# Optimization experiments

Hardware: AMD Instinct MI355X
Metric: run time of the kernel (lower is better)

Reference implementation:

```python
import jax, jax.numpy as jnp
import numpy as np

B, S, D, H, DFF = 2, 2048, 1024, 16, 4096
DK = D // H


def _layer_norm(x, g, b, eps=1e-5):
    mu = jnp.mean(x, axis=-1, keepdims=True)
    var = jnp.mean((x - mu) ** 2, axis=-1, keepdims=True)
    return (x - mu) / jnp.sqrt(var + eps) * g + b


def setup_inputs() -> dict:
    key = jax.random.key(0)
    ks = jax.random.split(key, 12)
    w = lambda k, shape: jax.random.normal(k, shape, jnp.float32) * 0.02
    return {
        "x": jax.random.normal(ks[0], (B, S, D), jnp.float32),
        "mask": jnp.tril(jnp.ones((1, 1, S, S), jnp.int32)),  # causal tgt mask
        "Wq": w(ks[1], (D, D)), "bq": jnp.zeros((D,), jnp.float32),
        "Wk": w(ks[2], (D, D)), "bk": jnp.zeros((D,), jnp.float32),
        "Wv": w(ks[3], (D, D)), "bv": jnp.zeros((D,), jnp.float32),
        "Wo": w(ks[4], (D, D)), "bo": jnp.zeros((D,), jnp.float32),
        "W1": w(ks[5], (D, DFF)), "b1": jnp.zeros((DFF,), jnp.float32),
        "W2": w(ks[6], (DFF, D)), "b2": jnp.zeros((D,), jnp.float32),
        "g1": jnp.ones((D,), jnp.float32), "be1": jnp.zeros((D,), jnp.float32),
        "g2": jnp.ones((D,), jnp.float32), "be2": jnp.zeros((D,), jnp.float32),
    }


def reference(x, mask, Wq, bq, Wk, bk, Wv, bv, Wo, bo, W1, b1, W2, b2, g1, be1, g2, be2):
    b, s, d = x.shape
    h, dk = H, DK
    split = lambda t: t.reshape(b, s, h, dk).transpose(0, 2, 1, 3)  # [b,h,s,dk]
    q = split(x @ Wq + bq)
    k = split(x @ Wk + bk)
    v = split(x @ Wv + bv)
    scores = jnp.einsum("bhqd,bhkd->bhqk", q, k) / jnp.sqrt(jnp.float32(dk))
    # ALiBi: slope_h = (2**(8/H))**-(h+1); bias[h,i,j] = slope_h * (j - i)
    slopes = (2.0 ** (8.0 / h)) ** (-jnp.arange(1, h + 1, dtype=jnp.float32))
    rel = (jnp.arange(s)[None, :] - jnp.arange(s)[:, None]).astype(jnp.float32)
    scores = scores + slopes[:, None, None] * rel[None]  # [1? broadcast b,h,s,s]
    scores = jnp.where(mask == 0, jnp.float32(-1e9), scores)
    probs = jax.nn.softmax(scores, axis=-1)
    attn = jnp.einsum("bhqk,bhkd->bhqd", probs, v)
    attn = attn.transpose(0, 2, 1, 3).reshape(b, s, d) @ Wo + bo
    x = _layer_norm(x + attn, g1, be1)
    ff = jax.nn.relu(x @ W1 + b1) @ W2 + b2
    return _layer_norm(x + ff, g2, be2)
```

## Files before the change

### kernel.cpp

```cpp
#include <hip/hip_runtime.h>
#include <stdint.h>

typedef unsigned short u16;
typedef __bf16 bf16x8 __attribute__((ext_vector_type(8)));
typedef float f32x4 __attribute__((ext_vector_type(4)));
typedef float f32x16 __attribute__((ext_vector_type(16)));
typedef unsigned int uint2v __attribute__((ext_vector_type(2)));

#define S_LEN 2048
#define D_MODEL 1024

struct TrueT  { static constexpr bool value = true;  };
struct FalseT { static constexpr bool value = false; };

__device__ __forceinline__ u16 f2b(float f) {
    uint32_t u = __float_as_uint(f);
    u += 0x7FFFu + ((u >> 16) & 1u);
    return (u16)(u >> 16);
}

__device__ __forceinline__ uint32_t pk2(float a, float b) {
    union { struct { __bf16 l, h; } s; uint32_t u; } c;
    c.s.l = (__bf16)a; c.s.h = (__bf16)b; return c.u;
}

__device__ __forceinline__ float fexp2(float x) {
#if __has_builtin(__builtin_amdgcn_exp2f)
    return __builtin_amdgcn_exp2f(x);
#else
    return exp2f(x);
#endif
}

__device__ __forceinline__ uint2v plswap(uint32_t a, uint32_t b) {
#if __has_builtin(__builtin_amdgcn_permlane32_swap)
    return __builtin_amdgcn_permlane32_swap(a, b, false, false);
#else
    uint2v r;
    uint32_t pa = (uint32_t)__shfl_xor((int)a, 32, 64);
    uint32_t pb = (uint32_t)__shfl_xor((int)b, 32, 64);
    const int hi = (threadIdx.x & 63) >> 5;
    r[0] = hi ? pb : a;
    r[1] = hi ? b : pa;
    return r;
#endif
}
__device__ __forceinline__ float xhalf_max(float x) {
    uint2v r = plswap(__float_as_uint(x), __float_as_uint(x));
    return fmaxf(__uint_as_float(r[0]), __uint_as_float(r[1]));
}
__device__ __forceinline__ float xhalf_add(float x) {
    uint2v r = plswap(__float_as_uint(x), __float_as_uint(x));
    return __uint_as_float(r[0]) + __uint_as_float(r[1]);
}

__device__ __forceinline__ void gl16(const void* g, void* l) {
    __builtin_amdgcn_global_load_lds(
        (const __attribute__((address_space(1))) void*)g,
        (__attribute__((address_space(3))) void*)l, 16, 0, 0);
}

__global__ __launch_bounds__(256) void k_convert_bf16(
    const float* __restrict__ in, u16* __restrict__ out, int n)
{
    int i = (blockIdx.x * 256 + threadIdx.x) * 4;
    if (i >= n) return;
    float4 v = *reinterpret_cast<const float4*>(in + i);
    ushort4 o;
    o.x = f2b(v.x); o.y = f2b(v.y); o.z = f2b(v.z); o.w = f2b(v.w);
    *reinterpret_cast<ushort4*>(out + i) = o;
}

__global__ __launch_bounds__(256) void k_transpose_w(
    const float* __restrict__ W, u16* __restrict__ WT, int K, int N)
{
    __shared__ float tile[32][33];
    const int nt = blockIdx.x, kt = blockIdx.y;
    const int tx = threadIdx.x & 31, ty = threadIdx.x >> 5;
#pragma unroll
    for (int i = 0; i < 4; ++i)
        tile[ty + i * 8][tx] = W[(long)(kt * 32 + ty + i * 8) * N + nt * 32 + tx];
    __syncthreads();
#pragma unroll
    for (int i = 0; i < 4; ++i)
        WT[(long)(nt * 32 + ty + i * 8) * K + kt * 32 + tx] = f2b(tile[tx][ty + i * 8]);
}

template <int MODE>
__global__ __launch_bounds__(256) void k_gemm(
    const u16* __restrict__ A, const u16* __restrict__ BT,
    const float* __restrict__ bias, const float* __restrict__ bias2,
    const float* __restrict__ bias3,
    u16* __restrict__ outb, float* __restrict__ outf,
    int M, int N, int K, int va, int vb)
{
    __shared__ u16 As[2][128 * 32];
    __shared__ u16 Bs[2][128 * 32];
    const int t = threadIdx.x;
    const int lane = t & 63, wid = t >> 6;
    const int wm = wid >> 1, wn = wid & 1;
    const int lr = lane & 15, lg = lane >> 4;

    const int GX = gridDim.x, GY = gridDim.y;
    const int dd = blockIdx.y * GX + blockIdx.x;
    const int xcd = dd & 7, ii = dd >> 3;
    const int hb = GY / va, wb = GX / vb;
    const int pr = xcd / vb, pc = xcd % vb;
    const int by = pr * hb + ii / wb;
    const int bx = pc * wb + ii % wb;
    const int m0 = by * 128, n0 = bx * 128;

    const int Kc = K / (int)gridDim.z;
    const long koff = (long)blockIdx.z * Kc;

    f32x4 acc[4][4];
#pragma unroll
    for (int i = 0; i < 4; ++i)
#pragma unroll
        for (int j = 0; j < 4; ++j) acc[i][j] = (f32x4){0.f, 0.f, 0.f, 0.f};

    const int r0 = t >> 2;
    const int ce = (t & 3) * 8;
    const u16* pA0 = A + (long)(m0 + r0) * K + ce + koff;
    const u16* pA1 = A + (long)(m0 + r0 + 64) * K + ce + koff;
    const u16* pB0 = BT + (long)(n0 + r0) * K + ce + koff;
    const u16* pB1 = BT + (long)(n0 + r0 + 64) * K + ce + koff;

    auto STAGE = [&](int buf, int k0) {
        u16* aw = &As[buf][wid * 512];
        u16* bw = &Bs[buf][wid * 512];
        gl16(pA0 + k0, aw);
        gl16(pA1 + k0, aw + 2048);
        gl16(pB0 + k0, bw);
        gl16(pB1 + k0, bw + 2048);
    };

    STAGE(0, 0);
    __syncthreads();
    int cur = 0;
    for (int k0 = 0; k0 < Kc; k0 += 32) {
        if (k0 + 32 < Kc) STAGE(cur ^ 1, k0 + 32);
        bf16x8 af[4], bfr[4];
#pragma unroll
        for (int i = 0; i < 4; ++i)
            af[i] = *reinterpret_cast<const bf16x8*>(&As[cur][(wm * 64 + i * 16 + lr) * 32 + lg * 8]);
#pragma unroll
        for (int j = 0; j < 4; ++j)
            bfr[j] = *reinterpret_cast<const bf16x8*>(&Bs[cur][(wn * 64 + j * 16 + lr) * 32 + lg * 8]);
#pragma unroll
        for (int i = 0; i < 4; ++i)
#pragma unroll
            for (int j = 0; j < 4; ++j)
                acc[i][j] = __builtin_amdgcn_mfma_f32_16x16x32_bf16(af[i], bfr[j], acc[i][j], 0, 0, 0);
        __syncthreads();
        cur ^= 1;
    }

    const long zoff = (long)blockIdx.z * M * N;
#pragma unroll
    for (int i = 0; i < 4; ++i) {
#pragma unroll
        for (int j = 0; j < 4; ++j) {
            const int n = n0 + wn * 64 + j * 16 + lr;
            float bn = 0.f;
            if (MODE == 0)
                bn = (n < 1024) ? bias[n] : (n < 2048) ? bias2[n - 1024] : bias3[n - 2048];
            else if (MODE == 2)
                bn = bias[n];
#pragma unroll
            for (int r = 0; r < 4; ++r) {
                const int m = m0 + wm * 64 + i * 16 + lg * 4 + r;
                float v = acc[i][j][r] + bn;
                if (MODE == 0) {
                    const int b = m >> 11, s = m & 2047;
                    const int which = n >> 10, nn = n & 1023;
                    const int h = nn >> 6, dk = nn & 63;
                    const long bhb = (long)(b * 16 + h) * (2048L * 64);
                    const int s32 = s >> 5, sr = s & 31;
                    long addr;
                    if (which < 2) {
                        addr = bhb + (long)s32 * 2048 + (dk >> 4) * 512 +
                               ((dk >> 3) & 1) * 256 + sr * 8 + (dk & 7);
                    } else {
                        addr = bhb + (long)s32 * 2048 + (dk >> 5) * 1024 +
                               ((sr >> 4) & 1) * 512 + ((sr >> 3) & 1) * 256 +
                               (dk & 31) * 8 + (sr & 7);
                    }
                    outb[(long)which * (32L * 2048 * 64) + addr] = f2b(v);
                } else if (MODE == 2) {
                    outb[(long)m * N + n] = f2b(fmaxf(v, 0.f));
                } else {
                    outf[zoff + (long)m * N + n] = v;
                }
            }
        }
    }
}

__global__ __launch_bounds__(512, 2) void k_gemm8(
    const u16* __restrict__ A, const u16* __restrict__ BT,
    const float* __restrict__ bias, u16* __restrict__ outb,
    int M, int N, int K, int va, int vb)
{
    __shared__ u16 As[2][2][8192];
    __shared__ u16 Bs[2][2][8192];
    const int t = threadIdx.x;
    const int lane = t & 63, wid = t >> 6;
    const int wm = wid >> 2, wn = wid & 3;
    const int lr = lane & 15, lg = lane >> 4;

    const int GX = gridDim.x, GY = gridDim.y;
    const int dd = blockIdx.y * GX + blockIdx.x;
    const int xcd = dd & 7, ii = dd >> 3;
    const int hb = GY / va, wb = GX / vb;
    const int by = (xcd / vb) * hb + ii / wb;
    const int bx = (xcd % vb) * wb + ii % wb;
    const int m0 = by * 256, n0 = bx * 256;

    const int NT = K >> 6;

    auto STAGEU = [&](const u16* __restrict__ P, int rbase, u16* lds_unit,
                      int tt, int kh) {
        const int ko = tt * 64 + kh * 32;
#pragma unroll
        for (int s = 0; s < 2; ++s) {
            const int c = wid * 64 + lane + s * 512;
            const int op = c * 16;
            const int row = op >> 6;
            const int kg = ((op >> 4) & 3) ^ ((row >> 1) & 3);
            gl16(P + (long)(rbase + row) * K + ko + kg * 8,
                 (char*)lds_unit + op);
        }
    };
    auto RD = [&](const u16* unit, int rb) -> bf16x8 {
        const int row = rb + lr;
        const int op = (row * 64 + lg * 16) ^ (((row >> 1) & 3) << 4);
        return *reinterpret_cast<const bf16x8*>((const char*)unit + op);
    };

    f32x4 acc[8][4];
#pragma unroll
    for (int i = 0; i < 8; ++i)
#pragma unroll
        for (int j = 0; j < 4; ++j) acc[i][j] = (f32x4){0.f, 0.f, 0.f, 0.f};

    STAGEU(A, m0, &As[0][0][0], 0, 0);
    STAGEU(BT, n0, &Bs[0][0][0], 0, 0);
    STAGEU(A, m0, &As[0][1][0], 0, 1);
    STAGEU(BT, n0, &Bs[0][1][0], 0, 1);
    STAGEU(A, m0, &As[1][0][0], 1, 0);
    STAGEU(BT, n0, &Bs[1][0][0], 1, 0);
    asm volatile("s_waitcnt vmcnt(0)" ::: "memory");
    __builtin_amdgcn_s_barrier();

    for (int tt = 0; tt < NT; ++tt) {
        const int sl = tt & 1;
        bf16x8 af[4], bfr[4];

#pragma unroll
        for (int rf = 0; rf < 4; ++rf)
            af[rf] = RD(&As[sl][0][0], wm * 128 + rf * 16);
#pragma unroll
        for (int cf = 0; cf < 4; ++cf)
            bfr[cf] = RD(&Bs[sl][0][0], wn * 64 + cf * 16);
        if (tt + 1 < NT) STAGEU(A, m0, &As[sl ^ 1][1][0], tt + 1, 1);
        __builtin_amdgcn_s_setprio(1);
#pragma unroll
        for (int cf = 0; cf < 4; ++cf)
#pragma unroll
            for (int rf = 0; rf < 4; ++rf)
                acc[rf][cf] = __builtin_amdgcn_mfma_f32_16x16x32_bf16(af[rf], bfr[cf], acc[rf][cf], 0, 0, 0);
        __builtin_amdgcn_s_setprio(0);
        __builtin_amdgcn_s_barrier();

#pragma unroll
        for (int rf = 0; rf < 4; ++rf)
            af[rf] = RD(&As[sl][0][0], wm * 128 + 64 + rf * 16);
        if (tt + 1 < NT) STAGEU(BT, n0, &Bs[sl ^ 1][1][0], tt + 1, 1);
        __builtin_amdgcn_s_setprio(1);
#pragma unroll
        for (int cf = 0; cf < 4; ++cf)
#pragma unroll
            for (int rf = 0; rf < 4; ++rf)
                acc[4 + rf][cf] = __builtin_amdgcn_mfma_f32_16x16x32_bf16(af[rf], bfr[cf], acc[4 + rf][cf], 0, 0, 0);
        __builtin_amdgcn_s_setprio(0);
        asm volatile("s_waitcnt vmcnt(8)" ::: "memory");
        __builtin_amdgcn_s_barrier();

#pragma unroll
        for (int rf = 0; rf < 4; ++rf)
            af[rf] = RD(&As[sl][1][0], wm * 128 + rf * 16);
#pragma unroll
        for (int cf = 0; cf < 4; ++cf)
            bfr[cf] = RD(&Bs[sl][1][0], wn * 64 + cf * 16);
        if (tt + 2 < NT) STAGEU(A, m0, &As[sl][0][0], tt + 2, 0);
        __builtin_amdgcn_s_setprio(1);
#pragma unroll
        for (int cf = 0; cf < 4; ++cf)
#pragma unroll
            for (int rf = 0; rf < 4; ++rf)
                acc[rf][cf] = __builtin_amdgcn_mfma_f32_16x16x32_bf16(af[rf], bfr[cf], acc[rf][cf], 0, 0, 0);
        __builtin_amdgcn_s_setprio(0);
        __builtin_amdgcn_s_barrier();

#pragma unroll
        for (int rf = 0; rf < 4; ++rf)
            af[rf] = RD(&As[sl][1][0], wm * 128 + 64 + rf * 16);
        if (tt + 2 < NT) STAGEU(BT, n0, &Bs[sl][0][0], tt + 2, 0);
        __builtin_amdgcn_s_setprio(1);
#pragma unroll
        for (int cf = 0; cf < 4; ++cf)
#pragma unroll
            for (int rf = 0; rf < 4; ++rf)
                acc[4 + rf][cf] = __builtin_amdgcn_mfma_f32_16x16x32_bf16(af[rf], bfr[cf], acc[4 + rf][cf], 0, 0, 0);
        __builtin_amdgcn_s_setprio(0);
        asm volatile("s_waitcnt vmcnt(8)" ::: "memory");
        __builtin_amdgcn_s_barrier();
    }

#pragma unroll
    for (int fr = 0; fr < 8; ++fr)
#pragma unroll
        for (int cf = 0; cf < 4; ++cf) {
            const int n = n0 + wn * 64 + cf * 16 + lr;
            const float bn = bias[n];
#pragma unroll
            for (int r = 0; r < 4; ++r) {
                const int m = m0 + wm * 128 + fr * 16 + lg * 4 + r;
                outb[(long)m * N + n] = f2b(fmaxf(acc[fr][cf][r] + bn, 0.f));
            }
        }
}

__global__ __launch_bounds__(512, 2) void k_gemm8n(
    const u16* __restrict__ A, const u16* __restrict__ BT,
    float* __restrict__ outf, int M, int N, int K, int va, int vb)
{
    __shared__ u16 As[2][2][8192];
    __shared__ u16 Bs[2][2][4096];
    const int t = threadIdx.x;
    const int lane = t & 63, wid = t >> 6;
    const int wm = wid >> 1, wn = wid & 1;
    const int lr = lane & 15, lg = lane >> 4;

    const int GX = gridDim.x, GY = gridDim.y;
    const int dd = blockIdx.y * GX + blockIdx.x;
    const int xcd = dd & 7, ii = dd >> 3;
    const int hb = GY / va, wb = GX / vb;
    const int by = (xcd / vb) * hb + ii / wb;
    const int bx = (xcd % vb) * wb + ii % wb;
    const int m0 = by * 256, n0 = bx * 128;

    const int Kc = K / (int)gridDim.z;
    const long koff = (long)blockIdx.z * Kc;
    const int NT = Kc >> 6;

    auto STAGEA = [&](u16* lds_unit, int tt, int kh) {
        const int ko = tt * 64 + kh * 32;
#pragma unroll
        for (int s = 0; s < 2; ++s) {
            const int c = wid * 64 + lane + s * 512;
            const int op = c * 16;
            const int row = op >> 6;
            const int kg = ((op >> 4) & 3) ^ ((row >> 1) & 3);
            gl16(A + (long)(m0 + row) * K + koff + ko + kg * 8,
                 (char*)lds_unit + op);
        }
    };
    auto STAGEB = [&](u16* lds_unit, int tt, int kh) {
        const int ko = tt * 64 + kh * 32;
        const int c = wid * 64 + lane;
        const int op = c * 16;
        const int row = op >> 6;
        const int kg = ((op >> 4) & 3) ^ ((row >> 1) & 3);
        gl16(BT + (long)(n0 + row) * K + koff + ko + kg * 8,
             (char*)lds_unit + op);
    };
    auto RD = [&](const u16* unit, int rb) -> bf16x8 {
        const int row = rb + lr;
        const int op = (row * 64 + lg * 16) ^ (((row >> 1) & 3) << 4);
        return *reinterpret_cast<const bf16x8*>((const char*)unit + op);
    };

    f32x4 acc[4][4];
#pragma unroll
    for (int i = 0; i < 4; ++i)
#pragma unroll
        for (int j = 0; j < 4; ++j) acc[i][j] = (f32x4){0.f, 0.f, 0.f, 0.f};

    STAGEA(&As[0][0][0], 0, 0); STAGEB(&Bs[0][0][0], 0, 0);
    STAGEA(&As[0][1][0], 0, 1); STAGEB(&Bs[0][1][0], 0, 1);
    STAGEA(&As[1][0][0], 1, 0); STAGEB(&Bs[1][0][0], 1, 0);
    asm volatile("s_waitcnt vmcnt(0)" ::: "memory");
    __builtin_amdgcn_s_barrier();

    for (int tt = 0; tt < NT; ++tt) {
        const int sl = tt & 1;
        bf16x8 af[4], bfr[4];

#pragma unroll
        for (int rf = 0; rf < 4; ++rf)
            af[rf] = RD(&As[sl][0][0], wm * 64 + rf * 16);
#pragma unroll
        for (int cf = 0; cf < 4; ++cf)
            bfr[cf] = RD(&Bs[sl][0][0], wn * 64 + cf * 16);
        if (tt + 1 < NT) {
            STAGEA(&As[sl ^ 1][1][0], tt + 1, 1);
            STAGEB(&Bs[sl ^ 1][1][0], tt + 1, 1);
        }
        __builtin_amdgcn_s_setprio(1);
#pragma unroll
        for (int cf = 0; cf < 4; ++cf)
#pragma unroll
            for (int rf = 0; rf < 4; ++rf)
                acc[rf][cf] = __builtin_amdgcn_mfma_f32_16x16x32_bf16(af[rf], bfr[cf], acc[rf][cf], 0, 0, 0);
        __builtin_amdgcn_s_setprio(0);
        asm volatile("s_waitcnt vmcnt(6)" ::: "memory");
        __builtin_amdgcn_s_barrier();

#pragma unroll
        for (int rf = 0; rf < 4; ++rf)
            af[rf] = RD(&As[sl][1][0], wm * 64 + rf * 16);
#pragma unroll
        for (int cf = 0; cf < 4; ++cf)
            bfr[cf] = RD(&Bs[sl][1][0], wn * 64 + cf * 16);
        if (tt + 2 < NT) {
            STAGEA(&As[sl][0][0], tt + 2, 0);
            STAGEB(&Bs[sl][0][0], tt + 2, 0);
        }
        __builtin_amdgcn_s_setprio(1);
#pragma unroll
        for (int cf = 0; cf < 4; ++cf)
#pragma unroll
            for (int rf = 0; rf < 4; ++rf)
                acc[rf][cf] = __builtin_amdgcn_mfma_f32_16x16x32_bf16(af[rf], bfr[cf], acc[rf][cf], 0, 0, 0);
        __builtin_amdgcn_s_setprio(0);
        asm volatile("s_waitcnt vmcnt(6)" ::: "memory");
        __builtin_amdgcn_s_barrier();
    }

    const long zoff = (long)blockIdx.z * M * N;
#pragma unroll
    for (int fr = 0; fr < 4; ++fr)
#pragma unroll
        for (int cf = 0; cf < 4; ++cf) {
            const int n = n0 + wn * 64 + cf * 16 + lr;
#pragma unroll
            for (int r = 0; r < 4; ++r) {
                const int m = m0 + wm * 64 + fr * 16 + lg * 4 + r;
                outf[zoff + (long)m * N + n] = acc[fr][cf][r];
            }
        }
}

__global__ __launch_bounds__(256, 3) void k_attn4(
    const u16* __restrict__ qg, const u16* __restrict__ kg,
    const u16* __restrict__ vtg, u16* __restrict__ attnb)
{
    __shared__ float Ol[4][32][68];
    __shared__ float Ml[4][32];
    __shared__ float Ll[4][32];

    const int t = threadIdx.x;
    const int lane = t & 63, w = t >> 6;
    const int qc = lane & 31, hi = lane >> 5;
    const int bid = blockIdx.x;
    const int xcd = bid & 7, slot = bid >> 3;
    const int bh = xcd * 4 + (slot & 3);
    const int pr = slot >> 2;
    const int b = bh >> 4, h = bh & 15;
    const float slope2 = fexp2(-0.5f * (float)(h + 1)) * 1.44269504f;
    const float SC = 0.18033688f;
    const long base = (long)bh * (S_LEN * 64L);

    const u16* kptr = kg + base + lane * 8;
    const u16* vptr = vtg + base + lane * 8;
    const u16* qptr = qg + base + lane * 8;

#define LOADK(S, DST) {                                                   \
        const u16* kr_ = kptr + (long)(S) * 2048;                         \
        DST[0] = *reinterpret_cast<const bf16x8*>(kr_);                   \
        DST[1] = *reinterpret_cast<const bf16x8*>(kr_ + 512);             \
        DST[2] = *reinterpret_cast<const bf16x8*>(kr_ + 1024);            \
        DST[3] = *reinterpret_cast<const bf16x8*>(kr_ + 1536); }

    for (int pi = 0; pi < 2; ++pi) {
        const int qt = pi ? pr : 63 - pr;
        const int q_abs = qt * 32 + qc;

        bf16x8 qf[4];
        {
            const u16* qt_ = qptr + (long)qt * 2048;
#pragma unroll
            for (int ds = 0; ds < 4; ++ds)
                qf[ds] = *reinterpret_cast<const bf16x8*>(qt_ + ds * 512);
        }

        f32x16 oacc[2];
#pragma unroll
        for (int i = 0; i < 16; ++i) { oacc[0][i] = 0.f; oacc[1][i] = 0.f; }
        float m = -1e30f, l = 0.f;

        const int nsub = qt + 1;
        const int L = (nsub + 3) >> 2;
        const int s_beg = w * L;
        const int s_end = min(s_beg + L, nsub);
        const bool has_diag = (s_beg < s_end) && (s_end == nsub);
        const int e_un = has_diag ? s_end - 1 : s_end;

        bf16x8 kf[4];

        auto SUBTILE = [&](int s, int nxt, auto MASKC) {
            constexpr bool MASK = decltype(MASKC)::value;
            const int k0 = s * 32;
            f32x16 st;
#pragma unroll
            for (int i = 0; i < 16; ++i) st[i] = 0.f;
#pragma unroll
            for (int ds = 0; ds < 4; ++ds)
                st = __builtin_amdgcn_mfma_f32_32x32x16_bf16(kf[ds], qf[ds], st, 0, 0, 0);
            if (nxt >= 0) LOADK(nxt, kf);
            bf16x8 vf[2][2];
            {
                const u16* vt_ = vptr + (long)s * 2048;
#pragma unroll
                for (int dh = 0; dh < 2; ++dh)
#pragma unroll
                    for (int ks = 0; ks < 2; ++ks)
                        vf[dh][ks] = *reinterpret_cast<const bf16x8*>(
                            vt_ + dh * 1024 + ks * 512);
            }

            const float b0 = slope2 * (float)(k0 - q_abs + 4 * hi);
#pragma unroll
            for (int r = 0; r < 16; ++r) {
                const int roff = (r & 3) + 8 * (r >> 2);
                float xx = fmaf(st[r], SC, fmaf((float)roff, slope2, b0));
                if (MASK) {
                    const int kabs = k0 + roff + 4 * hi;
                    xx = (kabs > q_abs) ? -1e30f : xx;
                }
                st[r] = xx;
            }
            float mt[8];
#pragma unroll
            for (int r = 0; r < 8; ++r) mt[r] = fmaxf(st[2 * r], st[2 * r + 1]);
#pragma unroll
            for (int r = 0; r < 4; ++r) mt[r] = fmaxf(mt[r], mt[r + 4]);
            mt[0] = fmaxf(mt[0], mt[2]); mt[1] = fmaxf(mt[1], mt[3]);
            float mloc = xhalf_max(fmaxf(mt[0], mt[1]));

            if (!__all(mloc <= m + 11.5416f)) {
                const float mnew = fmaxf(m, mloc);
                const float corr = fexp2(m - mnew);
                m = mnew;
                l *= corr;
#pragma unroll
                for (int i = 0; i < 16; ++i) { oacc[0][i] *= corr; oacc[1][i] *= corr; }
            }

#pragma unroll
            for (int r = 0; r < 16; ++r) st[r] = fexp2(st[r] - m);
            float pt[8];
#pragma unroll
            for (int r = 0; r < 8; ++r) pt[r] = st[2 * r] + st[2 * r + 1];
#pragma unroll
            for (int r = 0; r < 4; ++r) pt[r] = pt[r] + pt[r + 4];
            pt[0] += pt[2]; pt[1] += pt[3];
            l += xhalf_add(pt[0] + pt[1]);

            bf16x8 pa[2];
#pragma unroll
            for (int g2 = 0; g2 < 2; ++g2) {
                uint32_t o0 = pk2(st[8 * g2 + 0], st[8 * g2 + 1]);
                uint32_t o1 = pk2(st[8 * g2 + 2], st[8 * g2 + 3]);
                uint32_t o2 = pk2(st[8 * g2 + 4], st[8 * g2 + 5]);
                uint32_t o3 = pk2(st[8 * g2 + 6], st[8 * g2 + 7]);
                uint2v ra = plswap(o0, o2);
                uint2v rb = plswap(o1, o3);
                union { uint32_t wd[4]; bf16x8 v; } c;
                c.wd[0] = ra[0]; c.wd[1] = rb[0]; c.wd[2] = ra[1]; c.wd[3] = rb[1];
                pa[g2] = c.v;
            }
#pragma unroll
            for (int ks = 0; ks < 2; ++ks)
#pragma unroll
                for (int dh = 0; dh < 2; ++dh)
                    oacc[dh] = __builtin_amdgcn_mfma_f32_32x32x16_bf16(vf[dh][ks], pa[ks], oacc[dh], 0, 0, 0);
        };

        int s = s_beg;
        if (s < s_end) LOADK(s, kf);
        for (; s < e_un; ++s)
            SUBTILE(s, (s + 1 < s_end) ? s + 1 : -1, FalseT{});
        if (has_diag)
            SUBTILE(qt, -1, TrueT{});

#pragma unroll
        for (int dh = 0; dh < 2; ++dh)
#pragma unroll
            for (int g = 0; g < 4; ++g) {
                float4 o4 = make_float4(oacc[dh][4 * g + 0], oacc[dh][4 * g + 1],
                                        oacc[dh][4 * g + 2], oacc[dh][4 * g + 3]);
                *reinterpret_cast<float4*>(&Ol[w][qc][dh * 32 + g * 8 + hi * 4]) = o4;
            }
        if (hi == 0) { Ml[w][qc] = m; Ll[w][qc] = l; }
        __syncthreads();

        {
            const int q = t >> 3, dg = t & 7;
            const float m0v = Ml[0][q], m1v = Ml[1][q], m2v = Ml[2][q], m3v = Ml[3][q];
            const float M = fmaxf(fmaxf(m0v, m1v), fmaxf(m2v, m3v));
            float wgt[4];
            wgt[0] = fexp2(m0v - M); wgt[1] = fexp2(m1v - M);
            wgt[2] = fexp2(m2v - M); wgt[3] = fexp2(m3v - M);
            const float lsum = wgt[0] * Ll[0][q] + wgt[1] * Ll[1][q] +
                               wgt[2] * Ll[2][q] + wgt[3] * Ll[3][q];
            float acc8[8];
#pragma unroll
            for (int e = 0; e < 8; ++e) acc8[e] = 0.f;
#pragma unroll
            for (int w4 = 0; w4 < 4; ++w4) {
                const float wg = wgt[w4];
#pragma unroll
                for (int e = 0; e < 8; ++e)
                    acc8[e] += wg * Ol[w4][q][dg * 8 + e];
            }
            const float inv = 1.0f / lsum;
            u16 ob[8];
#pragma unroll
            for (int e = 0; e < 8; ++e) ob[e] = f2b(acc8[e] * inv);
            *reinterpret_cast<uint4*>(
                &attnb[((long)b * S_LEN + qt * 32 + q) * 1024 + h * 64 + dg * 8]) =
                *reinterpret_cast<uint4*>(&ob[0]);
        }
        __syncthreads();
    }
#undef LOADK
}

__global__ __launch_bounds__(256) void k_ln(
    const float* __restrict__ P0, const float* __restrict__ P1,
    const float* __restrict__ resid, const float* __restrict__ pbias,
    const float* __restrict__ g, const float* __restrict__ be,
    float* __restrict__ outf, u16* __restrict__ outb, int writeb)
{
    __shared__ float red[2][4];
    const int row = blockIdx.x, t = threadIdx.x;
    const long o = (long)row * 1024 + t * 4;
    float4 a0 = *reinterpret_cast<const float4*>(P0 + o);
    float4 a1 = *reinterpret_cast<const float4*>(P1 + o);
    float4 rr = *reinterpret_cast<const float4*>(resid + o);
    float4 pb = *reinterpret_cast<const float4*>(pbias + t * 4);
    float4 vv;
    vv.x = a0.x + a1.x + rr.x + pb.x;
    vv.y = a0.y + a1.y + rr.y + pb.y;
    vv.z = a0.z + a1.z + rr.z + pb.z;
    vv.w = a0.w + a1.w + rr.w + pb.w;
    float s = vv.x + vv.y + vv.z + vv.w;
    float sq = vv.x * vv.x + vv.y * vv.y + vv.z * vv.z + vv.w * vv.w;
#pragma unroll
    for (int off = 1; off < 64; off <<= 1) {
        s += __shfl_xor(s, off, 64);
        sq += __shfl_xor(sq, off, 64);
    }
    const int w = t >> 6;
    if ((t & 63) == 0) { red[0][w] = s; red[1][w] = sq; }
    __syncthreads();
    s = red[0][0] + red[0][1] + red[0][2] + red[0][3];
    sq = red[1][0] + red[1][1] + red[1][2] + red[1][3];
    const float mu = s * (1.f / 1024.f);
    const float var = sq * (1.f / 1024.f) - mu * mu;
    const float rs = rsqrtf(var + 1e-5f);
    float4 gv = *reinterpret_cast<const float4*>(&g[t * 4]);
    float4 bv = *reinterpret_cast<const float4*>(&be[t * 4]);
    float4 ov;
    ov.x = (vv.x - mu) * rs * gv.x + bv.x;
    ov.y = (vv.y - mu) * rs * gv.y + bv.y;
    ov.z = (vv.z - mu) * rs * gv.z + bv.z;
    ov.w = (vv.w - mu) * rs * gv.w + bv.w;
    *reinterpret_cast<float4*>(&outf[o]) = ov;
    if (writeb) {
        ushort4 ob;
        ob.x = f2b(ov.x); ob.y = f2b(ov.y); ob.z = f2b(ov.z); ob.w = f2b(ov.w);
        *reinterpret_cast<ushort4*>(&outb[o]) = ob;
    }
}

extern "C" void kernel_launch(void* const* d_in, const int* in_sizes, int n_in,
                              void* d_out, int out_size, void* d_ws, size_t ws_size,
                              hipStream_t stream)
{
    const float* x  = (const float*)d_in[0];
    const float* Wq = (const float*)d_in[2];  const float* bq = (const float*)d_in[3];
    const float* Wk = (const float*)d_in[4];  const float* bk = (const float*)d_in[5];
    const float* Wv = (const float*)d_in[6];  const float* bv = (const float*)d_in[7];
    const float* Wo = (const float*)d_in[8];  const float* bo = (const float*)d_in[9];
    const float* W1 = (const float*)d_in[10]; const float* b1 = (const float*)d_in[11];
    const float* W2 = (const float*)d_in[12]; const float* b2 = (const float*)d_in[13];
    const float* g1 = (const float*)d_in[14]; const float* be1 = (const float*)d_in[15];
    const float* g2 = (const float*)d_in[16]; const float* be2 = (const float*)d_in[17];
    float* out = (float*)d_out;

    char* ws = (char*)d_ws;
    const size_t MB = 1 << 20;
    u16* XB   = (u16*)(ws + 0 * MB);
    u16* QKVT = (u16*)(ws + 8 * MB);
    u16* WOT  = (u16*)(ws + 14 * MB);
    u16* W1T  = (u16*)(ws + 16 * MB);
    u16* W2T  = (u16*)(ws + 96 * MB);
    u16* QKV  = (u16*)(ws + 32 * MB);
    u16* AT   = (u16*)(ws + 64 * MB);
    float* OP = (float*)(ws + 32 * MB);
    float* Y1 = (float*)(ws + 0 * MB);
    u16* Y1B  = (u16*)(ws + 64 * MB);
    u16* Hb   = (u16*)(ws + 24 * MB);
    float* FP = (float*)(ws + 56 * MB);

    u16* Qb = QKV;
    u16* Kb = QKV + 32L * 2048 * 64;
    u16* Vb = QKV + 2 * 32L * 2048 * 64;

    dim3 blk(256);

    k_convert_bf16<<<dim3(4096), blk, 0, stream>>>(x, XB, 4096 * 1024);
    k_transpose_w<<<dim3(32, 32), blk, 0, stream>>>(Wq, QKVT, 1024, 1024);
    k_transpose_w<<<dim3(32, 32), blk, 0, stream>>>(Wk, QKVT + 1024L * 1024, 1024, 1024);
    k_transpose_w<<<dim3(32, 32), blk, 0, stream>>>(Wv, QKVT + 2048L * 1024, 1024, 1024);
    k_transpose_w<<<dim3(32, 32), blk, 0, stream>>>(Wo, WOT, 1024, 1024);
    k_transpose_w<<<dim3(128, 32), blk, 0, stream>>>(W1, W1T, 1024, 4096);
    k_transpose_w<<<dim3(32, 128), blk, 0, stream>>>(W2, W2T, 4096, 1024);

    k_gemm<0><<<dim3(24, 32), blk, 0, stream>>>(XB, QKVT, bq, bk, bv,
                                                QKV, nullptr, 4096, 3072, 1024, 4, 2);

    k_attn4<<<dim3(1024), blk, 0, stream>>>(Qb, Kb, Vb, AT);

    k_gemm8n<<<dim3(8, 16, 2), dim3(512), 0, stream>>>(AT, WOT, OP,
                                                       4096, 1024, 1024, 2, 4);
    k_ln<<<dim3(4096), blk, 0, stream>>>(OP, OP + 4096L * 1024, x, bo,
                                         g1, be1, Y1, Y1B, 1);
    k_gemm8<<<dim3(16, 16), dim3(512), 0, stream>>>(Y1B, W1T, b1, Hb,
                                                    4096, 4096, 1024, 2, 4);
    k_gemm8n<<<dim3(8, 16, 2), dim3(512), 0, stream>>>(Hb, W2T, FP,
                                                       4096, 1024, 4096, 2, 4);
    k_ln<<<dim3(4096), blk, 0, stream>>>(FP, FP + 4096L * 1024, Y1, b2,
                                         g2, be2, out, nullptr, 0);
}
```

Measured before the change: 222.9 us.

## Use 256x256 split-K=4 GEMM for FFN down-projection with bf16 partials

The W2 GEMM moves from the 256x128 split-K=2 kernel to the 256x256 tile kernel, now templated to support split-K over gridDim.z. It writes four bf16 partial planes with no bias. A new LayerNorm kernel sums the four bf16 partials with the residual and bias before normalizing. The aim is better operand reuse from the larger tile, plus half-width partial traffic in exchange for extra partial planes, at the cost of precision loss from rounding the partials to bf16.

```diff
diff --git a/kernel.cpp b/kernel.cpp
--- a/kernel.cpp
+++ b/kernel.cpp
@@ -17,6 +17,11 @@
     uint32_t u = __float_as_uint(f);
     u += 0x7FFFu + ((u >> 16) & 1u);
     return (u16)(u >> 16);
+}
+
+__device__ __forceinline__ float b2f(u16 b) {
+    uint32_t u = (uint32_t)b << 16;
+    return __uint_as_float(u);
 }
 
 __device__ __forceinline__ uint32_t pk2(float a, float b) {
@@ -197,6 +202,7 @@
     }
 }
 
+template <int MODE>
 __global__ __launch_bounds__(512, 2) void k_gemm8(
     const u16* __restrict__ A, const u16* __restrict__ BT,
     const float* __restrict__ bias, u16* __restrict__ outb,
@@ -217,7 +223,9 @@
     const int bx = (xcd % vb) * wb + ii % wb;
     const int m0 = by * 256, n0 = bx * 256;
 
-    const int NT = K >> 6;
+    const int Kc = K / (int)gridDim.z;
+    const long koff = (long)blockIdx.z * Kc;
+    const int NT = Kc >> 6;
 
     auto STAGEU = [&](const u16* __restrict__ P, int rbase, u16* lds_unit,
                       int tt, int kh) {
@@ -228,7 +236,7 @@
             const int op = c * 16;
             const int row = op >> 6;
             const int kg = ((op >> 4) & 3) ^ ((row >> 1) & 3);
-            gl16(P + (long)(rbase + row) * K + ko + kg * 8,
+            gl16(P + (long)(rbase + row) * K + koff + ko + kg * 8,
                  (char*)lds_unit + op);
         }
     };
@@ -318,16 +326,20 @@
         __builtin_amdgcn_s_barrier();
     }
 
+    const long zoff = (long)blockIdx.z * M * N;
 #pragma unroll
     for (int fr = 0; fr < 8; ++fr)
 #pragma unroll
         for (int cf = 0; cf < 4; ++cf) {
             const int n = n0 + wn * 64 + cf * 16 + lr;
-            const float bn = bias[n];
+            const float bn = (MODE == 0) ? bias[n] : 0.f;
 #pragma unroll
             for (int r = 0; r < 4; ++r) {
                 const int m = m0 + wm * 128 + fr * 16 + lg * 4 + r;
-                outb[(long)m * N + n] = f2b(fmaxf(acc[fr][cf][r] + bn, 0.f));
+                if (MODE == 0)
+                    outb[(long)m * N + n] = f2b(fmaxf(acc[fr][cf][r] + bn, 0.f));
+                else
+                    outb[zoff + (long)m * N + n] = f2b(acc[fr][cf][r]);
             }
         }
 }
@@ -687,6 +699,51 @@
     }
 }
 
+__global__ __launch_bounds__(256) void k_ln4b(
+    const u16* __restrict__ P, long plane,
+    const float* __restrict__ resid, const float* __restrict__ pbias,
+    const float* __restrict__ g, const float* __restrict__ be,
+    float* __restrict__ outf)
+{
+    __shared__ float red[2][4];
+    const int row = blockIdx.x, t = threadIdx.x;
+    const long o = (long)row * 1024 + t * 4;
+    float4 rr = *reinterpret_cast<const float4*>(resid + o);
+    float4 pb = *reinterpret_cast<const float4*>(pbias + t * 4);
+    float4 vv;
+    vv.x = rr.x + pb.x; vv.y = rr.y + pb.y;
+    vv.z = rr.z + pb.z; vv.w = rr.w + pb.w;
+#pragma unroll
+    for (int z = 0; z < 4; ++z) {
+        ushort4 p4 = *reinterpret_cast<const ushort4*>(P + z * plane + o);
+        vv.x += b2f(p4.x); vv.y += b2f(p4.y);
+        vv.z += b2f(p4.z); vv.w += b2f(p4.w);
+    }
+    float s = vv.x + vv.y + vv.z + vv.w;
+    float sq = vv.x * vv.x + vv.y * vv.y + vv.z * vv.z + vv.w * vv.w;
+#pragma unroll
+    for (int off = 1; off < 64; off <<= 1) {
+        s += __shfl_xor(s, off, 64);
+        sq += __shfl_xor(sq, off, 64);
+    }
+    const int w = t >> 6;
+    if ((t & 63) == 0) { red[0][w] = s; red[1][w] = sq; }
+    __syncthreads();
+    s = red[0][0] + red[0][1] + red[0][2] + red[0][3];
+    sq = red[1][0] + red[1][1] + red[1][2] + red[1][3];
+    const float mu = s * (1.f / 1024.f);
+    const float var = sq * (1.f / 1024.f) - mu * mu;
+    const float rs = rsqrtf(var + 1e-5f);
+    float4 gv = *reinterpret_cast<const float4*>(&g[t * 4]);
+    float4 bv = *reinterpret_cast<const float4*>(&be[t * 4]);
+    float4 ov;
+    ov.x = (vv.x - mu) * rs * gv.x + bv.x;
+    ov.y = (vv.y - mu) * rs * gv.y + bv.y;
+    ov.z = (vv.z - mu) * rs * gv.z + bv.z;
+    ov.w = (vv.w - mu) * rs * gv.w + bv.w;
+    *reinterpret_cast<float4*>(&outf[o]) = ov;
+}
+
 extern "C" void kernel_launch(void* const* d_in, const int* in_sizes, int n_in,
                               void* d_out, int out_size, void* d_ws, size_t ws_size,
                               hipStream_t stream)
@@ -715,7 +772,7 @@
     float* Y1 = (float*)(ws + 0 * MB);
     u16* Y1B  = (u16*)(ws + 64 * MB);
     u16* Hb   = (u16*)(ws + 24 * MB);
-    float* FP = (float*)(ws + 56 * MB);
+    u16* FPB  = (u16*)(ws + 56 * MB);
 
     u16* Qb = QKV;
     u16* Kb = QKV + 32L * 2048 * 64;
@@ -740,10 +797,10 @@
                                                        4096, 1024, 1024, 2, 4);
     k_ln<<<dim3(4096), blk, 0, stream>>>(OP, OP + 4096L * 1024, x, bo,
                                          g1, be1, Y1, Y1B, 1);
-    k_gemm8<<<dim3(16, 16), dim3(512), 0, stream>>>(Y1B, W1T, b1, Hb,
-                                                    4096, 4096, 1024, 2, 4);
-    k_gemm8n<<<dim3(8, 16, 2), dim3(512), 0, stream>>>(Hb, W2T, FP,
-                                                       4096, 1024, 4096, 2, 4);
-    k_ln<<<dim3(4096), blk, 0, stream>>>(FP, FP + 4096L * 1024, Y1, b2,
-                                         g2, be2, out, nullptr, 0);
-}
+    k_gemm8<0><<<dim3(16, 16), dim3(512), 0, stream>>>(Y1B, W1T, b1, Hb,
+                                                       4096, 4096, 1024, 2, 4);
+    k_gemm8<1><<<dim3(4, 16, 4), dim3(512), 0, stream>>>(Hb, W2T, nullptr, FPB,
+                                                         4096, 1024, 4096, 4, 2);
+    k_ln4b<<<dim3(4096), blk, 0, stream>>>(FPB, 4096L * 1024, Y1, b2,
+                                           g2, be2, out);
+}
```

New measurement: 220.3 us, median of 3. Within noise of the previous version (-1.2%).
